# Kernel optimization log

Measured on AMD Instinct MI355X. Metric: run time of the kernel, lower is better.

The kernel has to match this reference:

```python
import jax, jax.numpy as jnp
import numpy as np
from jax import lax

B, C, H, W = 16, 64, 160, 160
K, O, KS = 8, 64, 3
A = 16  # attention_channel = max(int(64*0.0625), 16)
EPS = 1e-5


def setup_inputs() -> dict:
    key = jax.random.key(0)
    ks = jax.random.split(key, 16)
    return {
        'x': jax.random.normal(ks[0], (B, C, H, W), jnp.float32),
        'scale': jnp.ones((2,), jnp.float32) * 2.0,  # (scale_h, scale_w)
        'rw1': jax.random.normal(ks[1], (2 * C, C + 2), jnp.float32) * 0.1,
        'rb1': jnp.zeros((2 * C,), jnp.float32),
        'rw2': jax.random.normal(ks[2], (C, 2 * C), jnp.float32) * 0.1,
        'rb2': jnp.zeros((C,), jnp.float32),
        'fc_w': jax.random.normal(ks[3], (A, C), jnp.float32) * 0.1,
        'bn_gamma': jnp.ones((A,), jnp.float32),
        'bn_beta': jnp.zeros((A,), jnp.float32),
        'bn_mean': jax.random.normal(ks[4], (A,), jnp.float32) * 0.1,
        'bn_var': jax.random.uniform(ks[5], (A,), jnp.float32, 0.5, 1.5),
        'cfc_w': jax.random.normal(ks[6], (C, A), jnp.float32) * 0.1,
        'cfc_b': jnp.zeros((C,), jnp.float32),
        'ffc_w': jax.random.normal(ks[7], (O, A), jnp.float32) * 0.1,
        'ffc_b': jnp.zeros((O,), jnp.float32),
        'sfc_w': jax.random.normal(ks[8], (KS * KS, A), jnp.float32) * 0.1,
        'sfc_b': jnp.zeros((KS * KS,), jnp.float32),
        'kfc_w': jax.random.normal(ks[9], (K, A), jnp.float32) * 0.1,
        'kfc_b': jnp.zeros((K,), jnp.float32),
        'weight': jax.random.normal(ks[10], (K, O, C, KS, KS), jnp.float32) * 0.05,
    }


def reference(x, scale, rw1, rb1, rw2, rb2, fc_w, bn_gamma, bn_beta, bn_mean,
              bn_var, cfc_w, cfc_b, ffc_w, ffc_b, sfc_w, sfc_b, kfc_w, kfc_b,
              weight):
    b, c, h, w = x.shape
    k_num, o, cg, ks, _ = weight.shape
    # scale routing MLP: concat [1/sh, 1/sw, GAP(x)] -> relu(Linear) -> relu(Linear)
    gap = x.mean(axis=(2, 3))  # [B, C]
    scale_info = jnp.broadcast_to(1.0 / scale, (b, 2))
    s = jnp.concatenate([scale_info, gap], axis=1)  # [B, C+2]
    s = jax.nn.relu(s @ rw1.T + rb1)
    routed = jax.nn.relu(s @ rw2.T + rb2)  # [B, C]
    # ScaleAttention trunk: 1x1 conv (no bias) + BN(eval) + ReLU on [B,C,1,1]
    v = routed @ fc_w.T  # [B, A]
    v = (v - bn_mean) * lax.rsqrt(bn_var + EPS) * bn_gamma + bn_beta
    v = jax.nn.relu(v)
    # four attention heads (temperature = 1.0)
    channel_att = jax.nn.sigmoid(v @ cfc_w.T + cfc_b)            # [B, C]
    filter_att = jax.nn.sigmoid(v @ ffc_w.T + ffc_b)             # [B, O]
    spatial_att = jax.nn.sigmoid(v @ sfc_w.T + sfc_b).reshape(b, 1, 1, 1, ks, ks)
    kernel_att = jax.nn.softmax(v @ kfc_w.T + kfc_b, axis=1).reshape(b, k_num, 1, 1, 1, 1)
    # channel-gate input, aggregate per-sample dynamic kernels over experts
    xc = x * channel_att[:, :, None, None]
    agg_w = jnp.sum(spatial_att * kernel_att * weight[None], axis=1)  # [B,O,C,ks,ks]
    agg_w = agg_w.reshape(b * o, cg, ks, ks)
    # grouped-conv trick: groups = batch (original groups=1)
    out = lax.conv_general_dilated(
        xc.reshape(1, b * c, h, w), agg_w,
        window_strides=(1, 1), padding=((1, 1), (1, 1)),
        feature_group_count=b,
        dimension_numbers=('NCHW', 'OIHW', 'NCHW'))
    out = out.reshape(b, o, h, w) * filter_att[:, :, None, None]
    return out
```

## Files before the change

### kernel.cpp

```cpp
#include <hip/hip_runtime.h>
#include <math.h>

#define BB 16
#define CC 64
#define HH 160
#define WW 160
#define KK 8
#define OO 64
#define AA 16
#define HWQ (HH * WW)

typedef __attribute__((ext_vector_type(8))) short sh8;
typedef __attribute__((ext_vector_type(4))) float fx4;

__device__ inline unsigned short f2bf(float f) {
    unsigned int u = __float_as_uint(f);
    return (unsigned short)((u + 0x7FFFu + ((u >> 16) & 1u)) >> 16);
}
__device__ inline float bf2f(unsigned short h) {
    return __uint_as_float(((unsigned int)h) << 16);
}

__global__ __launch_bounds__(256) void trans_gap_kernel(
    const float* __restrict__ x,
    unsigned short* __restrict__ xt_hi, unsigned short* __restrict__ xt_lo,
    float* __restrict__ gap) {
    __shared__ float ts[64][33];
    const int w0 = blockIdx.x * 32;
    const int h  = blockIdx.y;
    const int b  = blockIdx.z;
    const int tid = threadIdx.x;

    for (int i = tid; i < 2048; i += 256) {
        int c = i >> 5, wi = i & 31;
        ts[c][wi] = x[(((size_t)b * CC + c) * HH + h) * WW + w0 + wi];
    }
    __syncthreads();
    if (tid < 64) {
        float s = 0.f;
        #pragma unroll 8
        for (int wi = 0; wi < 32; ++wi) s += ts[tid][wi];
        atomicAdd(&gap[b * CC + tid], s);
    }
    for (int i = tid; i < 2048; i += 256) {
        int c = i & 63, w = i >> 6;
        float v = ts[c][w];
        unsigned short hi = f2bf(v);
        unsigned short lo = f2bf(v - bf2f(hi));
        size_t off = (((size_t)(b * HH + h)) * WW + w0 + w) * CC + c;
        xt_hi[off] = hi;
        xt_lo[off] = lo;
    }
}

__global__ __launch_bounds__(128) void mlp_kernel(
    const float* __restrict__ scale,
    const float* __restrict__ rw1, const float* __restrict__ rb1,
    const float* __restrict__ rw2, const float* __restrict__ rb2,
    const float* __restrict__ fc_w,
    const float* __restrict__ bn_gamma, const float* __restrict__ bn_beta,
    const float* __restrict__ bn_mean, const float* __restrict__ bn_var,
    const float* __restrict__ cfc_w, const float* __restrict__ cfc_b,
    const float* __restrict__ ffc_w, const float* __restrict__ ffc_b,
    const float* __restrict__ sfc_w, const float* __restrict__ sfc_b,
    const float* __restrict__ kfc_w, const float* __restrict__ kfc_b,
    const float* __restrict__ gap,
    float* __restrict__ ca, float* __restrict__ fa,
    float* __restrict__ sa, float* __restrict__ ka) {
    int b = blockIdx.x;
    int t = threadIdx.x;
    __shared__ float sin_[CC + 2];
    __shared__ float h1[2 * CC];
    __shared__ float h2[CC];
    __shared__ float vv[AA];
    __shared__ float kl[KK];

    if (t < 2) sin_[t] = 1.0f / scale[t];
    else if (t < CC + 2) sin_[t] = gap[b * CC + (t - 2)] * (1.0f / (float)HWQ);
    __syncthreads();

    {
        float a = rb1[t];
        const float* wr = rw1 + (size_t)t * (CC + 2);
        #pragma unroll 6
        for (int j = 0; j < CC + 2; ++j) a += sin_[j] * wr[j];
        h1[t] = fmaxf(a, 0.f);
    }
    __syncthreads();

    if (t < CC) {
        float a = rb2[t];
        const float* wr = rw2 + (size_t)t * (2 * CC);
        #pragma unroll 8
        for (int j = 0; j < 2 * CC; ++j) a += h1[j] * wr[j];
        h2[t] = fmaxf(a, 0.f);
    }
    __syncthreads();

    if (t < AA) {
        float a = 0.f;
        const float* wr = fc_w + (size_t)t * CC;
        #pragma unroll 8
        for (int j = 0; j < CC; ++j) a += h2[j] * wr[j];
        a = (a - bn_mean[t]) * rsqrtf(bn_var[t] + 1e-5f) * bn_gamma[t] + bn_beta[t];
        vv[t] = fmaxf(a, 0.f);
    }
    __syncthreads();

    if (t < CC) {
        float a = cfc_b[t];
        const float* wr = cfc_w + (size_t)t * AA;
        #pragma unroll
        for (int j = 0; j < AA; ++j) a += vv[j] * wr[j];
        ca[b * CC + t] = 1.f / (1.f + expf(-a));
        float f = ffc_b[t];
        const float* wf = ffc_w + (size_t)t * AA;
        #pragma unroll
        for (int j = 0; j < AA; ++j) f += vv[j] * wf[j];
        fa[b * CC + t] = 1.f / (1.f + expf(-f));
    }
    if (t < 9) {
        float a = sfc_b[t];
        const float* wr = sfc_w + (size_t)t * AA;
        #pragma unroll
        for (int j = 0; j < AA; ++j) a += vv[j] * wr[j];
        sa[b * 16 + t] = 1.f / (1.f + expf(-a));
    }
    if (t < KK) {
        float a = kfc_b[t];
        const float* wr = kfc_w + (size_t)t * AA;
        #pragma unroll
        for (int j = 0; j < AA; ++j) a += vv[j] * wr[j];
        kl[t] = a;
    }
    __syncthreads();
    if (t < KK) {
        float m = kl[0];
        #pragma unroll
        for (int j = 1; j < KK; ++j) m = fmaxf(m, kl[j]);
        float sum = 0.f;
        #pragma unroll
        for (int j = 0; j < KK; ++j) sum += expf(kl[j] - m);
        ka[b * KK + t] = expf(kl[t] - m) / sum;
    }
}

__global__ __launch_bounds__(256) void agg_frag_kernel(
    const float* __restrict__ weight,
    const float* __restrict__ ca, const float* __restrict__ fa,
    const float* __restrict__ sa, const float* __restrict__ ka,
    unsigned short* __restrict__ Ahi, unsigned short* __restrict__ Alo) {
    int e = blockIdx.x * 256 + threadIdx.x;
    int q  = e % 9;
    int t2 = e / 9;
    int c  = t2 & 63;
    int bo = t2 >> 6;
    int o  = bo & 63;
    int b  = bo >> 6;
    float s = 0.f;
    #pragma unroll
    for (int k = 0; k < KK; ++k)
        s += ka[b * KK + k] * weight[(((size_t)(k * OO + o)) * CC + c) * 9 + q];
    float val = s * sa[b * 16 + q] * ca[b * CC + c] * fa[b * CC + o];
    unsigned short hi = f2bf(val);
    unsigned short lo = f2bf(val - bf2f(hi));
    int mt = o >> 4;
    int lane = (o & 15) | (((c >> 3) & 3) << 4);
    int j = c & 7;
    int ch = c >> 5;
    size_t off = ((((size_t)(b * 9 + q) * 2 + ch) * 4 + mt) * 64 + lane) * 8 + j;
    Ahi[off] = hi;
    Alo[off] = lo;
}

__global__ __launch_bounds__(256) void conv_mfma_kernel(
    const unsigned short* __restrict__ xt_hi,
    const unsigned short* __restrict__ xt_lo,
    const unsigned short* __restrict__ Ahi,
    const unsigned short* __restrict__ Alo,
    float* __restrict__ out) {
    __shared__ __align__(16) unsigned short xs_hi[6 * 18 * 64];
    __shared__ __align__(16) unsigned short xs_lo[6 * 18 * 64];

    const int b  = blockIdx.z;
    const int h0 = blockIdx.y * 4;
    const int w0 = blockIdx.x * 16;
    const int tid  = threadIdx.x;
    const int wv   = tid >> 6;
    const int lane = tid & 63;

    for (int i = tid; i < 6 * 18 * 8; i += 256) {
        int g   = i & 7;
        int col = (i >> 3) % 18;
        int row = i / (8 * 18);
        int gh = h0 - 1 + row;
        int gw = w0 - 1 + col;
        uint4 vhi = {0u, 0u, 0u, 0u}, vlo = {0u, 0u, 0u, 0u};
        if ((unsigned)gh < (unsigned)HH && (unsigned)gw < (unsigned)WW) {
            size_t off = (((size_t)(b * HH + gh)) * WW + gw) * CC + g * 8;
            vhi = *(const uint4*)(xt_hi + off);
            vlo = *(const uint4*)(xt_lo + off);
        }
        int lidx = (row * 18 + col) * 64 + ((g ^ (col & 7)) << 3);
        *(uint4*)(&xs_hi[lidx]) = vhi;
        *(uint4*)(&xs_lo[lidx]) = vlo;
    }
    __syncthreads();

    fx4 z = {0.f, 0.f, 0.f, 0.f};
    fx4 acc[4] = {z, z, z, z};

    const int lr  = lane & 15;
    const int l4  = lane >> 4;

    #pragma unroll
    for (int q = 0; q < 9; ++q) {
        const int kh = q / 3, kw = q % 3;
        const int row = wv + kh;
        const int col = lr + kw;
        const int lbase = (row * 18 + col) * 64;
        #pragma unroll
        for (int ch = 0; ch < 2; ++ch) {
            const int g = ch * 4 + l4;
            const int lidx = lbase + ((g ^ (col & 7)) << 3);
            sh8 bhi = *(const sh8*)(&xs_hi[lidx]);
            sh8 blo = *(const sh8*)(&xs_lo[lidx]);
            const size_t abase =
                ((size_t)((b * 9 + q) * 2 + ch) * 4) * 512 + lane * 8;
            #pragma unroll
            for (int mt = 0; mt < 4; ++mt) {
                sh8 a_hi = *(const sh8*)(Ahi + abase + mt * 512);
                sh8 a_lo = *(const sh8*)(Alo + abase + mt * 512);
                acc[mt] = __builtin_amdgcn_mfma_f32_16x16x32_bf16(
                    a_hi, bhi, acc[mt], 0, 0, 0);
                acc[mt] = __builtin_amdgcn_mfma_f32_16x16x32_bf16(
                    a_hi, blo, acc[mt], 0, 0, 0);
                acc[mt] = __builtin_amdgcn_mfma_f32_16x16x32_bf16(
                    a_lo, bhi, acc[mt], 0, 0, 0);
            }
        }
    }

    const int dw = lr;
    const int osub = l4 * 4;
    const int hrow = h0 + wv;
    #pragma unroll
    for (int mt = 0; mt < 4; ++mt) {
        #pragma unroll
        for (int jj = 0; jj < 4; ++jj) {
            int o = mt * 16 + osub + jj;
            out[((size_t)(b * OO + o)) * HWQ + hrow * WW + w0 + dw] = acc[mt][jj];
        }
    }
}

extern "C" void kernel_launch(void* const* d_in, const int* in_sizes, int n_in,
                              void* d_out, int out_size, void* d_ws, size_t ws_size,
                              hipStream_t stream) {
    const float* x        = (const float*)d_in[0];
    const float* scale    = (const float*)d_in[1];
    const float* rw1      = (const float*)d_in[2];
    const float* rb1      = (const float*)d_in[3];
    const float* rw2      = (const float*)d_in[4];
    const float* rb2      = (const float*)d_in[5];
    const float* fc_w     = (const float*)d_in[6];
    const float* bn_gamma = (const float*)d_in[7];
    const float* bn_beta  = (const float*)d_in[8];
    const float* bn_mean  = (const float*)d_in[9];
    const float* bn_var   = (const float*)d_in[10];
    const float* cfc_w    = (const float*)d_in[11];
    const float* cfc_b    = (const float*)d_in[12];
    const float* ffc_w    = (const float*)d_in[13];
    const float* ffc_b    = (const float*)d_in[14];
    const float* sfc_w    = (const float*)d_in[15];
    const float* sfc_b    = (const float*)d_in[16];
    const float* kfc_w    = (const float*)d_in[17];
    const float* kfc_b    = (const float*)d_in[18];
    const float* weight   = (const float*)d_in[19];

    const size_t WS_NEEDED = 107233280u;
    if (ws_size < WS_NEEDED) return;

    char* wsb = (char*)d_ws;
    float* gap = (float*)(wsb + 0);
    float* ca  = (float*)(wsb + 4096);
    float* fa  = (float*)(wsb + 8192);
    float* sa  = (float*)(wsb + 12288);
    float* ka  = (float*)(wsb + 13312);
    unsigned short* Ahi  = (unsigned short*)(wsb + 16384);
    unsigned short* Alo  = (unsigned short*)(wsb + 1196032);
    unsigned short* xthi = (unsigned short*)(wsb + 2375680);
    unsigned short* xtlo = (unsigned short*)(wsb + 54804480);

    hipMemsetAsync(gap, 0, 1024 * sizeof(float), stream);
    trans_gap_kernel<<<dim3(5, 160, 16), dim3(256), 0, stream>>>(
        x, xthi, xtlo, gap);
    mlp_kernel<<<dim3(BB), dim3(128), 0, stream>>>(
        scale, rw1, rb1, rw2, rb2, fc_w, bn_gamma, bn_beta, bn_mean, bn_var,
        cfc_w, cfc_b, ffc_w, ffc_b, sfc_w, sfc_b, kfc_w, kfc_b,
        gap, ca, fa, sa, ka);
    agg_frag_kernel<<<dim3(589824 / 256), dim3(256), 0, stream>>>(
        weight, ca, fa, sa, ka, Ahi, Alo);
    conv_mfma_kernel<<<dim3(10, 40, 16), dim3(256), 0, stream>>>(
        xthi, xtlo, Ahi, Alo, (float*)d_out);
}
```

Baseline: 402.7 us.

## Reuse conv weight fragments across two rows and vectorize input transpose

```diff
diff --git a/kernel.cpp b/kernel.cpp
--- a/kernel.cpp
+++ b/kernel.cpp
@@ -21,35 +21,47 @@
     return __uint_as_float(((unsigned int)h) << 16);
 }
 
-__global__ __launch_bounds__(256) void trans_gap_kernel(
+__global__ __launch_bounds__(256) void trans_kernel(
     const float* __restrict__ x,
     unsigned short* __restrict__ xt_hi, unsigned short* __restrict__ xt_lo,
-    float* __restrict__ gap) {
-    __shared__ float ts[64][33];
-    const int w0 = blockIdx.x * 32;
-    const int h  = blockIdx.y;
-    const int b  = blockIdx.z;
-    const int tid = threadIdx.x;
-
-    for (int i = tid; i < 2048; i += 256) {
-        int c = i >> 5, wi = i & 31;
-        ts[c][wi] = x[(((size_t)b * CC + c) * HH + h) * WW + w0 + wi];
-    }
-    __syncthreads();
+    float* __restrict__ pg) {
+    __shared__ float ts[64][84];
+    const int half = blockIdx.x;
+    const int h    = blockIdx.y;
+    const int b    = blockIdx.z;
+    const int w0   = half * 80;
+    const int tid  = threadIdx.x;
+
+    for (int i = tid; i < 1280; i += 256) {
+        int c  = i / 20;
+        int wq = i % 20;
+        float4 v = *(const float4*)(
+            x + (((size_t)(b * CC + c)) * HH + h) * WW + w0 + wq * 4);
+        *(float4*)(&ts[c][wq * 4]) = v;
+    }
+    __syncthreads();
+
     if (tid < 64) {
         float s = 0.f;
-        #pragma unroll 8
-        for (int wi = 0; wi < 32; ++wi) s += ts[tid][wi];
-        atomicAdd(&gap[b * CC + tid], s);
-    }
-    for (int i = tid; i < 2048; i += 256) {
-        int c = i & 63, w = i >> 6;
-        float v = ts[c][w];
-        unsigned short hi = f2bf(v);
-        unsigned short lo = f2bf(v - bf2f(hi));
-        size_t off = (((size_t)(b * HH + h)) * WW + w0 + w) * CC + c;
-        xt_hi[off] = hi;
-        xt_lo[off] = lo;
+        #pragma unroll 10
+        for (int w = 0; w < 80; ++w) s += ts[tid][w];
+        pg[((size_t)b * 320 + h * 2 + half) * 64 + tid] = s;
+    }
+
+    for (int i = tid; i < 640; i += 256) {
+        int g = i & 7;
+        int w = i >> 3;
+        sh8 vh, vl;
+        #pragma unroll
+        for (int e = 0; e < 8; ++e) {
+            float v = ts[g * 8 + e][w];
+            unsigned short hh = f2bf(v);
+            vh[e] = (short)hh;
+            vl[e] = (short)f2bf(v - bf2f(hh));
+        }
+        size_t off = (((size_t)(b * HH + h)) * WW + w0 + w) * CC + g * 8;
+        *(sh8*)(xt_hi + off) = vh;
+        *(sh8*)(xt_lo + off) = vl;
     }
 }
 
@@ -64,7 +76,7 @@
     const float* __restrict__ ffc_w, const float* __restrict__ ffc_b,
     const float* __restrict__ sfc_w, const float* __restrict__ sfc_b,
     const float* __restrict__ kfc_w, const float* __restrict__ kfc_b,
-    const float* __restrict__ gap,
+    const float* __restrict__ pg,
     float* __restrict__ ca, float* __restrict__ fa,
     float* __restrict__ sa, float* __restrict__ ka) {
     int b = blockIdx.x;
@@ -76,7 +88,12 @@
     __shared__ float kl[KK];
 
     if (t < 2) sin_[t] = 1.0f / scale[t];
-    else if (t < CC + 2) sin_[t] = gap[b * CC + (t - 2)] * (1.0f / (float)HWQ);
+    if (t < CC) {
+        float s = 0.f;
+        for (int h2v = 0; h2v < 320; ++h2v)
+            s += pg[((size_t)b * 320 + h2v) * 64 + t];
+        sin_[2 + t] = s * (1.0f / (float)HWQ);
+    }
     __syncthreads();
 
     {
@@ -179,20 +196,20 @@
     const unsigned short* __restrict__ Ahi,
     const unsigned short* __restrict__ Alo,
     float* __restrict__ out) {
-    __shared__ __align__(16) unsigned short xs_hi[6 * 18 * 64];
-    __shared__ __align__(16) unsigned short xs_lo[6 * 18 * 64];
+    __shared__ __align__(16) unsigned short xs_hi[10 * 18 * 64];
+    __shared__ __align__(16) unsigned short xs_lo[10 * 18 * 64];
 
     const int b  = blockIdx.z;
-    const int h0 = blockIdx.y * 4;
+    const int h0 = blockIdx.y * 8;
     const int w0 = blockIdx.x * 16;
     const int tid  = threadIdx.x;
     const int wv   = tid >> 6;
     const int lane = tid & 63;
 
-    for (int i = tid; i < 6 * 18 * 8; i += 256) {
+    for (int i = tid; i < 10 * 18 * 8; i += 256) {
         int g   = i & 7;
         int col = (i >> 3) % 18;
-        int row = i / (8 * 18);
+        int row = i / 144;
         int gh = h0 - 1 + row;
         int gw = w0 - 1 + col;
         uint4 vhi = {0u, 0u, 0u, 0u}, vlo = {0u, 0u, 0u, 0u};
@@ -208,48 +225,57 @@
     __syncthreads();
 
     fx4 z = {0.f, 0.f, 0.f, 0.f};
-    fx4 acc[4] = {z, z, z, z};
-
-    const int lr  = lane & 15;
-    const int l4  = lane >> 4;
+    fx4 acc[2][4] = {{z, z, z, z}, {z, z, z, z}};
+
+    const int lr = lane & 15;
+    const int l4 = lane >> 4;
 
     #pragma unroll
     for (int q = 0; q < 9; ++q) {
         const int kh = q / 3, kw = q % 3;
-        const int row = wv + kh;
         const int col = lr + kw;
-        const int lbase = (row * 18 + col) * 64;
         #pragma unroll
         for (int ch = 0; ch < 2; ++ch) {
-            const int g = ch * 4 + l4;
-            const int lidx = lbase + ((g ^ (col & 7)) << 3);
-            sh8 bhi = *(const sh8*)(&xs_hi[lidx]);
-            sh8 blo = *(const sh8*)(&xs_lo[lidx]);
+            const int g  = ch * 4 + l4;
+            const int cg = (g ^ (col & 7)) << 3;
+            sh8 bhi[2], blo[2];
+            #pragma unroll
+            for (int nr = 0; nr < 2; ++nr) {
+                const int row  = wv * 2 + nr + kh;
+                const int lidx = (row * 18 + col) * 64 + cg;
+                bhi[nr] = *(const sh8*)(&xs_hi[lidx]);
+                blo[nr] = *(const sh8*)(&xs_lo[lidx]);
+            }
             const size_t abase =
-                ((size_t)((b * 9 + q) * 2 + ch) * 4) * 512 + lane * 8;
+                ((size_t)((b * 9 + q) * 2 + ch)) * 2048 + lane * 8;
             #pragma unroll
             for (int mt = 0; mt < 4; ++mt) {
                 sh8 a_hi = *(const sh8*)(Ahi + abase + mt * 512);
                 sh8 a_lo = *(const sh8*)(Alo + abase + mt * 512);
-                acc[mt] = __builtin_amdgcn_mfma_f32_16x16x32_bf16(
-                    a_hi, bhi, acc[mt], 0, 0, 0);
-                acc[mt] = __builtin_amdgcn_mfma_f32_16x16x32_bf16(
-                    a_hi, blo, acc[mt], 0, 0, 0);
-                acc[mt] = __builtin_amdgcn_mfma_f32_16x16x32_bf16(
-                    a_lo, bhi, acc[mt], 0, 0, 0);
+                #pragma unroll
+                for (int nr = 0; nr < 2; ++nr) {
+                    acc[nr][mt] = __builtin_amdgcn_mfma_f32_16x16x32_bf16(
+                        a_hi, bhi[nr], acc[nr][mt], 0, 0, 0);
+                    acc[nr][mt] = __builtin_amdgcn_mfma_f32_16x16x32_bf16(
+                        a_hi, blo[nr], acc[nr][mt], 0, 0, 0);
+                    acc[nr][mt] = __builtin_amdgcn_mfma_f32_16x16x32_bf16(
+                        a_lo, bhi[nr], acc[nr][mt], 0, 0, 0);
+                }
             }
         }
     }
 
-    const int dw = lr;
-    const int osub = l4 * 4;
-    const int hrow = h0 + wv;
     #pragma unroll
-    for (int mt = 0; mt < 4; ++mt) {
-        #pragma unroll
-        for (int jj = 0; jj < 4; ++jj) {
-            int o = mt * 16 + osub + jj;
-            out[((size_t)(b * OO + o)) * HWQ + hrow * WW + w0 + dw] = acc[mt][jj];
+    for (int nr = 0; nr < 2; ++nr) {
+        const int hrow = h0 + wv * 2 + nr;
+        #pragma unroll
+        for (int mt = 0; mt < 4; ++mt) {
+            #pragma unroll
+            for (int jj = 0; jj < 4; ++jj) {
+                int o = mt * 16 + l4 * 4 + jj;
+                out[((size_t)(b * OO + o)) * HWQ + hrow * WW + w0 + lr] =
+                    acc[nr][mt][jj];
+            }
         }
     }
 }
@@ -282,25 +308,24 @@
     if (ws_size < WS_NEEDED) return;
 
     char* wsb = (char*)d_ws;
-    float* gap = (float*)(wsb + 0);
-    float* ca  = (float*)(wsb + 4096);
-    float* fa  = (float*)(wsb + 8192);
-    float* sa  = (float*)(wsb + 12288);
-    float* ka  = (float*)(wsb + 13312);
+    float* ca  = (float*)(wsb + 0);
+    float* fa  = (float*)(wsb + 4096);
+    float* sa  = (float*)(wsb + 8192);
+    float* ka  = (float*)(wsb + 12288);
+    float* pg  = (float*)(wsb + 16384);
     unsigned short* Ahi  = (unsigned short*)(wsb + 16384);
     unsigned short* Alo  = (unsigned short*)(wsb + 1196032);
     unsigned short* xthi = (unsigned short*)(wsb + 2375680);
     unsigned short* xtlo = (unsigned short*)(wsb + 54804480);
 
-    hipMemsetAsync(gap, 0, 1024 * sizeof(float), stream);
-    trans_gap_kernel<<<dim3(5, 160, 16), dim3(256), 0, stream>>>(
-        x, xthi, xtlo, gap);
+    trans_kernel<<<dim3(2, 160, 16), dim3(256), 0, stream>>>(
+        x, xthi, xtlo, pg);
     mlp_kernel<<<dim3(BB), dim3(128), 0, stream>>>(
         scale, rw1, rb1, rw2, rb2, fc_w, bn_gamma, bn_beta, bn_mean, bn_var,
         cfc_w, cfc_b, ffc_w, ffc_b, sfc_w, sfc_b, kfc_w, kfc_b,
-        gap, ca, fa, sa, ka);
+        pg, ca, fa, sa, ka);
     agg_frag_kernel<<<dim3(589824 / 256), dim3(256), 0, stream>>>(
         weight, ca, fa, sa, ka, Ahi, Alo);
-    conv_mfma_kernel<<<dim3(10, 40, 16), dim3(256), 0, stream>>>(
+    conv_mfma_kernel<<<dim3(10, 20, 16), dim3(256), 0, stream>>>(
         xthi, xtlo, Ahi, Alo, (float*)d_out);
 }
```

Result: faster. 340.3 us (-15.5%).
